# Kernel optimization log

Hardware: AMD Instinct MI355X
Metric: run time of the kernel (lower is better)

## Reference

```python
import jax, jax.numpy as jnp
import numpy as np

N_NODES = 102400   # 256 graphs x 400 nodes
N_EDGES = 1638400  # avg degree 16
C_IN = 128
C_OUT = 128
N_SAGE = 3         # gnn_num
G = 256            # num graphs
M = 400            # nodes per graph (equal-sized -> to_dense_batch is a reshape)


def setup_inputs() -> dict:
    key = jax.random.key(0)
    ks = jax.random.split(key, 6)
    x = jax.random.normal(ks[0], (N_NODES, C_IN), dtype=jnp.float32)
    edge_index = jax.random.randint(ks[1], (2, N_EDGES), 0, N_NODES, dtype=jnp.int32)
    # nodes sorted by graph id, equal graph sizes (matches to_dense_batch assumptions)
    batch = (jnp.arange(N_NODES, dtype=jnp.int32) // M)
    s_in = 1.0 / np.sqrt(C_IN)
    s_out = 1.0 / np.sqrt(C_OUT)
    W_g = jax.random.normal(ks[2], (C_IN, C_OUT), dtype=jnp.float32) * s_in
    b_g = jnp.zeros((C_OUT,), dtype=jnp.float32)
    W_l = jax.random.normal(ks[3], (N_SAGE, C_OUT, C_OUT), dtype=jnp.float32) * s_out  # neighbor lin
    b_l = jnp.zeros((N_SAGE, C_OUT), dtype=jnp.float32)
    W_r = jax.random.normal(ks[4], (N_SAGE, C_OUT, C_OUT), dtype=jnp.float32) * s_out  # root lin (no bias in PyG)
    return {"x": x, "W_g": W_g, "b_g": b_g, "W_l": W_l, "b_l": b_l,
            "W_r": W_r, "edge_index": edge_index, "batch": batch}


def _gcn_conv(x, W, b, src, dst):
    # PyG GCNConv: h = x W; add self loops; norm = d^{-1/2}_src * d^{-1/2}_dst,
    # deg = in-degree at dst counting the self loop; aggregate at dst; add bias.
    h = x @ W                                                     # [N, C_out]
    ones = jnp.ones((N_EDGES,), dtype=h.dtype)
    deg = jax.ops.segment_sum(ones, dst, num_segments=N_NODES) + 1.0
    dinv = jax.lax.rsqrt(deg)                                     # [N]
    norm = dinv[src] * dinv[dst]                                  # [E]
    agg = jax.ops.segment_sum(h[src] * norm[:, None], dst, num_segments=N_NODES)
    agg = agg + h * (dinv * dinv)[:, None]                        # self-loop term
    return agg + b


def _sage_conv(x, W_l, b_l, W_r, src, dst):
    # PyG SAGEConv (mean aggr): out = mean_{j in N(i)} x_j @ W_l + b_l + x @ W_r
    ones = jnp.ones((N_EDGES,), dtype=x.dtype)
    cnt = jax.ops.segment_sum(ones, dst, num_segments=N_NODES)
    s = jax.ops.segment_sum(x[src], dst, num_segments=N_NODES)
    mean = s / jnp.maximum(cnt, 1.0)[:, None]
    return mean @ W_l + b_l + x @ W_r


def _to_dense(x):
    # equal-sized graphs with nodes sorted by batch -> to_dense_batch == reshape
    return x.reshape(G, M, C_OUT)


def reference(x, W_g, b_g, W_l, b_l, W_r, edge_index, batch):
    src, dst = edge_index[0], edge_index[1]
    x = jax.nn.relu(_gcn_conv(x, W_g, b_g, src, dst))
    outs = [_to_dense(x)]
    for i in range(N_SAGE):
        x = jax.nn.relu(_sage_conv(x, W_l[i], b_l[i], W_r[i], src, dst))
        outs.append(_to_dense(x))
    return jnp.stack(outs)  # [N_SAGE+1, G, M, C_OUT]
```

## Files before the change

kernel.cpp:

```cpp
#include <hip/hip_runtime.h>

#define C 128
#define SLOT 64
typedef __attribute__((ext_vector_type(8))) short bf16x8;
typedef __attribute__((ext_vector_type(4))) float f32x4;

__device__ __forceinline__ unsigned short f2bf_rtn(float f) {
    unsigned u = __float_as_uint(f);
    return (unsigned short)((u + 0x7fff + ((u >> 16) & 1)) >> 16);
}
__device__ __forceinline__ float bflo(unsigned u) { return __uint_as_float(u << 16); }
__device__ __forceinline__ float bfhi(unsigned u) { return __uint_as_float(u & 0xffff0000u); }

__device__ __forceinline__ void gload_lds16(const unsigned short* g, unsigned short* l) {
    __builtin_amdgcn_global_load_lds(
        (const __attribute__((address_space(1))) void*)g,
        (__attribute__((address_space(3))) void*)l, 16, 0, 0);
}


__global__ void deg_fill_kernel(const int* __restrict__ ei, int* __restrict__ deg,
                                int* __restrict__ csr, int E) {
    int e = blockIdx.x * blockDim.x + threadIdx.x;
    if (e < E) {
        int d = ei[E + e];
        int r = atomicAdd(&deg[d], 1);
        if (r < SLOT) csr[(d << 6) + r] = ei[e];
    }
}

__global__ void prep_kernel(const int* __restrict__ deg, float* __restrict__ dinv,
                            float* __restrict__ cinv, int n) {
    int i = blockIdx.x * blockDim.x + threadIdx.x;
    if (i < n) {
        int d = deg[i];
        dinv[i] = rsqrtf((float)(d + 1));
        cinv[i] = 1.0f / (float)max(d, 1);
    }
}


__device__ __forceinline__ void split_bf16(float w, unsigned short& hb, unsigned short& lb) {
    unsigned u = __float_as_uint(w);
    hb = (unsigned short)(u >> 16);
    float hf = __uint_as_float(u & 0xffff0000u);
    lb = (unsigned short)(__float_as_uint(w - hf) >> 16);
}

__global__ __launch_bounds__(256) void wprep_gcn(const float* __restrict__ Wg,
                                                 unsigned short* __restrict__ dst) {
    int idx = blockIdx.x * 256 + threadIdx.x;
    if (idx >= 2 * 128 * 64) return;
    int k64 = idx & 63, ch = (idx >> 6) & 127, chunk = idx >> 13;
    int k = chunk * 64 + k64;
    unsigned short hb, lb;
    split_bf16(Wg[(size_t)k * 128 + ch], hb, lb);
    int pos = (((k64 >> 3) ^ (ch & 7)) << 3) | (k64 & 7);
    size_t base = ((size_t)chunk * 2) * 8192 + ch * 64 + pos;
    dst[base] = hb;
    dst[base + 8192] = lb;
}

__global__ __launch_bounds__(256) void wprep_fused(const float* __restrict__ Wl,
        const float* __restrict__ Wr, unsigned short* __restrict__ dst) {
    int idx = blockIdx.x * 256 + threadIdx.x;
    if (idx >= 3 * 4 * 128 * 64) return;
    int k64 = idx & 63, ch = (idx >> 6) & 127, chunk = (idx >> 13) & 3, layer = idx >> 15;
    int k = chunk * 64 + k64;
    float w = (k < 128) ? Wl[((size_t)layer * 128 + k) * 128 + ch]
                        : Wr[((size_t)layer * 128 + (k - 128)) * 128 + ch];
    unsigned short hb, lb;
    split_bf16(w, hb, lb);
    int pos = (((k64 >> 3) ^ (ch & 7)) << 3) | (k64 & 7);
    size_t base = (((size_t)layer * 4 + chunk) * 2) * 8192 + ch * 64 + pos;
    dst[base] = hb;
    dst[base + 8192] = lb;
}

template<int FUSED, int WBF>
__global__ __launch_bounds__(256) void gemm_mfma(
        const float* __restrict__ A0f, const unsigned short* __restrict__ Mbf,
        const unsigned short* __restrict__ Wp, const float* __restrict__ bias,
        float* __restrict__ outf, unsigned short* __restrict__ outbf) {
    const int NCHUNK = FUSED ? 4 : 2;
    __shared__ unsigned short Bs[2][128][64];
    unsigned short* BsFlat = &Bs[0][0][0];
    const int t = threadIdx.x;
    const int lane = t & 63;
    const int wv = t >> 6;
    const int rowbase = blockIdx.x * 64 + wv * 16;
    const int arow = rowbase + (lane & 15);
    const int kq = lane >> 4;

    f32x4 acc[8];
#pragma unroll
    for (int f = 0; f < 8; f++) acc[f] = (f32x4){0.f, 0.f, 0.f, 0.f};

#pragma unroll
    for (int c = 0; c < NCHUNK; c++) {
        __syncthreads();
        {
            const unsigned short* srcW = Wp + (size_t)c * 16384;
#pragma unroll
            for (int i = 0; i < 8; i++)
                gload_lds16(srcW + (wv * 8 + i) * 512 + lane * 8,
                            BsFlat + (wv * 8 + i) * 512);
        }
        const bool mside = (FUSED && c < 2);
        bf16x8 Ah[2], Al[2];
#pragma unroll
        for (int j = 0; j < 2; j++) {
            if (mside) {
                Ah[j] = *(const bf16x8*)(Mbf + (size_t)arow * C + c * 64 + j * 32 + kq * 8);
            } else {
                const int kb = (FUSED ? (c - 2) : c) * 64 + j * 32;
                const float* base = A0f + (size_t)arow * C + kb;
                float4 x0 = ((const float4*)base)[kq * 2];
                float4 x1 = ((const float4*)base)[kq * 2 + 1];
                float xv[8] = {x0.x, x0.y, x0.z, x0.w, x1.x, x1.y, x1.z, x1.w};
#pragma unroll
                for (int q = 0; q < 8; q++) {
                    unsigned u = __float_as_uint(xv[q]);
                    Ah[j][q] = (short)(u >> 16);
                    float hf = __uint_as_float(u & 0xffff0000u);
                    Al[j][q] = (short)(__float_as_uint(xv[q] - hf) >> 16);
                }
            }
        }
        __syncthreads();
#pragma unroll
        for (int j = 0; j < 2; j++) {
#pragma unroll
            for (int f = 0; f < 8; f++) {
                const int chh = f * 16 + (lane & 15);
                const int uu = (j * 4 + kq) ^ (lane & 7);
                bf16x8 bh = *(const bf16x8*)&Bs[0][chh][uu * 8];
                bf16x8 bl = *(const bf16x8*)&Bs[1][chh][uu * 8];
                acc[f] = __builtin_amdgcn_mfma_f32_16x16x32_bf16(Ah[j], bh, acc[f], 0, 0, 0);
                if (!mside)
                    acc[f] = __builtin_amdgcn_mfma_f32_16x16x32_bf16(Al[j], bh, acc[f], 0, 0, 0);
                acc[f] = __builtin_amdgcn_mfma_f32_16x16x32_bf16(Ah[j], bl, acc[f], 0, 0, 0);
            }
        }
    }
    const int col = lane & 15;
    const int rq = lane >> 4;
    if (FUSED) {
#pragma unroll
        for (int f = 0; f < 8; f++) {
            const float b = bias[f * 16 + col];
#pragma unroll
            for (int j = 0; j < 4; j++) {
                const size_t o = (size_t)(rowbase + rq * 4 + j) * C + f * 16 + col;
                float v = fmaxf(acc[f][j] + b, 0.f);
                outf[o] = v;
                if (WBF) outbf[o] = f2bf_rtn(v);
            }
        }
    } else {
        float sc[4];
#pragma unroll
        for (int j = 0; j < 4; j++) sc[j] = bias[rowbase + rq * 4 + j];
#pragma unroll
        for (int f = 0; f < 8; f++)
#pragma unroll
            for (int j = 0; j < 4; j++) {
                const size_t o = (size_t)(rowbase + rq * 4 + j) * C + f * 16 + col;
                outbf[o] = f2bf_rtn(acc[f][j] * sc[j]);
            }
    }
}

template<int SELF, int BIASRELU, int WF, int WBF>
__global__ __launch_bounds__(256) void agg_kernel(
        const unsigned short* __restrict__ tbl, const int* __restrict__ csr,
        const int* __restrict__ deg, const float* __restrict__ scale,
        const float* __restrict__ bias, float* __restrict__ outf,
        unsigned short* __restrict__ outbf, int n) {
    const int lane = threadIdx.x & 63;
    const int half = lane >> 5, li = lane & 31;
    const int i = blockIdx.x * 8 + (threadIdx.x >> 6) * 2 + half;
    if (i >= n) return;
    const int dcount = min(deg[i], SLOT);
    const int b = i << 6;
    const int c4 = li * 4;
    float a0 = 0.f, a1 = 0.f, a2 = 0.f, a3 = 0.f;
    for (int base = 0; base < dcount; base += 32) {
        const int cnt = min(32, dcount - base);
        int idx = (base + li < dcount) ? csr[b + base + li] : 0;
        int p = 0;
        for (; p + 4 <= cnt; p += 4) {
            int s0 = __shfl(idx, half * 32 + p);
            int s1 = __shfl(idx, half * 32 + p + 1);
            int s2 = __shfl(idx, half * 32 + p + 2);
            int s3 = __shfl(idx, half * 32 + p + 3);
            uint2 v0 = *(const uint2*)(tbl + (size_t)s0 * C + c4);
            uint2 v1 = *(const uint2*)(tbl + (size_t)s1 * C + c4);
            uint2 v2 = *(const uint2*)(tbl + (size_t)s2 * C + c4);
            uint2 v3 = *(const uint2*)(tbl + (size_t)s3 * C + c4);
            a0 += bflo(v0.x) + bflo(v1.x) + bflo(v2.x) + bflo(v3.x);
            a1 += bfhi(v0.x) + bfhi(v1.x) + bfhi(v2.x) + bfhi(v3.x);
            a2 += bflo(v0.y) + bflo(v1.y) + bflo(v2.y) + bflo(v3.y);
            a3 += bfhi(v0.y) + bfhi(v1.y) + bfhi(v2.y) + bfhi(v3.y);
        }
        for (; p < cnt; p++) {
            int s = __shfl(idx, half * 32 + p);
            uint2 v = *(const uint2*)(tbl + (size_t)s * C + c4);
            a0 += bflo(v.x); a1 += bfhi(v.x);
            a2 += bflo(v.y); a3 += bfhi(v.y);
        }
    }
    if (SELF) {
        uint2 h = *(const uint2*)(tbl + (size_t)i * C + c4);
        a0 += bflo(h.x); a1 += bfhi(h.x);
        a2 += bflo(h.y); a3 += bfhi(h.y);
    }
    const float sc = scale[i];
    a0 *= sc; a1 *= sc; a2 *= sc; a3 *= sc;
    if (BIASRELU) {
        float4 bb = *(const float4*)(bias + c4);
        a0 = fmaxf(a0 + bb.x, 0.f);
        a1 = fmaxf(a1 + bb.y, 0.f);
        a2 = fmaxf(a2 + bb.z, 0.f);
        a3 = fmaxf(a3 + bb.w, 0.f);
    }
    if (WF) {
        float4 r; r.x = a0; r.y = a1; r.z = a2; r.w = a3;
        *(float4*)(outf + (size_t)i * C + c4) = r;
    }
    if (WBF) {
        uint2 pk;
        pk.x = (unsigned)f2bf_rtn(a0) | ((unsigned)f2bf_rtn(a1) << 16);
        pk.y = (unsigned)f2bf_rtn(a2) | ((unsigned)f2bf_rtn(a3) << 16);
        *(uint2*)(outbf + (size_t)i * C + c4) = pk;
    }
}


extern "C" void kernel_launch(void* const* d_in, const int* in_sizes, int n_in,
                              void* d_out, int out_size, void* d_ws, size_t ws_size,
                              hipStream_t stream) {
    const float* x   = (const float*)d_in[0];
    const float* W_g = (const float*)d_in[1];
    const float* b_g = (const float*)d_in[2];
    const float* W_l = (const float*)d_in[3];
    const float* b_l = (const float*)d_in[4];
    const float* W_r = (const float*)d_in[5];
    const int*   ei  = (const int*)d_in[6];

    const int N = in_sizes[0] / C;
    const int E = in_sizes[6] / 2;
    const size_t NC = (size_t)N * C;

    char* ws = (char*)d_ws;
    unsigned short* meanbf = (unsigned short*)ws;
    unsigned short* tblA   = meanbf + NC;
    unsigned short* tblB   = tblA + NC;
    int* deg  = (int*)(tblB + NC);
    float* dinv = (float*)(deg + N);
    float* cinv = dinv + N;
    unsigned short* wsWg = (unsigned short*)(cinv + N);
    unsigned short* wsWf = wsWg + 32768;

    float* out0 = (float*)d_out;
    int* csr = (int*)(out0 + 3 * NC);

    hipMemsetAsync(deg, 0, (size_t)N * 4, stream);
    deg_fill_kernel<<<(E + 255) / 256, 256, 0, stream>>>(ei, deg, csr, E);
    prep_kernel<<<(N + 255) / 256, 256, 0, stream>>>(deg, dinv, cinv, N);
    wprep_gcn<<<64, 256, 0, stream>>>(W_g, wsWg);
    wprep_fused<<<384, 256, 0, stream>>>(W_l, W_r, wsWf);

    gemm_mfma<0, 1><<<N / 64, 256, 0, stream>>>(x, nullptr, wsWg, dinv, nullptr, tblA);
    agg_kernel<1, 1, 1, 1><<<(N + 7) / 8, 256, 0, stream>>>(tblA, csr, deg, dinv,
                                                            b_g, out0, tblB, N);

    const unsigned short* tin[3] = {tblB, tblA, tblB};
    unsigned short* tout[3] = {tblA, tblB, nullptr};
    for (int l = 0; l < 3; l++) {
        const float* xin = out0 + (size_t)l * NC;
        float* yout      = out0 + (size_t)(l + 1) * NC;
        agg_kernel<0, 0, 0, 1><<<(N + 7) / 8, 256, 0, stream>>>(
            tin[l], csr, deg, cinv, nullptr, nullptr, meanbf, N);
        if (l < 2)
            gemm_mfma<1, 1><<<N / 64, 256, 0, stream>>>(xin, meanbf,
                wsWf + (size_t)l * 65536, b_l + (size_t)l * C, yout, tout[l]);
        else
            gemm_mfma<1, 0><<<N / 64, 256, 0, stream>>>(xin, meanbf,
                wsWf + (size_t)l * 65536, b_l + (size_t)l * C, yout, nullptr);
    }
}
```

Measured before the change: 481.6 us.

## Split CSR build into rank+scatter fused with GCN GEMM; read bf16 root features in SAGE GEMM

The degree-count kernel now records only each edge's atomic rank. The CSR scatter runs on the even blocks of a new kernel whose odd blocks compute the GCN linear transform, so the irregular scatter overlaps with MFMA work. The SAGE GEMM now takes the root features from the bf16 table already produced for aggregation, instead of reloading fp32 activations and splitting them into hi/lo parts. This removes one MFMA per step and half the activation read traffic, at the cost of bf16 precision on the root term.

New measurement: 456.1 us. -5.3%, faster.

```diff
diff --git a/kernel.cpp b/kernel.cpp
--- a/kernel.cpp
+++ b/kernel.cpp
@@ -19,14 +19,10 @@
 }
 
 
-__global__ void deg_fill_kernel(const int* __restrict__ ei, int* __restrict__ deg,
-                                int* __restrict__ csr, int E) {
+__global__ void deg_rank_kernel(const int* __restrict__ ei, int* __restrict__ deg,
+                                int* __restrict__ rank, int E) {
     int e = blockIdx.x * blockDim.x + threadIdx.x;
-    if (e < E) {
-        int d = ei[E + e];
-        int r = atomicAdd(&deg[d], 1);
-        if (r < SLOT) csr[(d << 6) + r] = ei[e];
-    }
+    if (e < E) rank[e] = atomicAdd(&deg[ei[E + e]], 1);
 }
 
 __global__ void prep_kernel(const int* __restrict__ deg, float* __restrict__ dinv,
@@ -77,12 +73,97 @@
     dst[base + 8192] = lb;
 }
 
-template<int FUSED, int WBF>
-__global__ __launch_bounds__(256) void gemm_mfma(
-        const float* __restrict__ A0f, const unsigned short* __restrict__ Mbf,
+__global__ __launch_bounds__(256) void csr_gemm_kernel(
+        const int* __restrict__ ei, const int* __restrict__ rank,
+        int* __restrict__ csr, int E,
+        const float* __restrict__ x, const unsigned short* __restrict__ Wp,
+        const float* __restrict__ dinv, unsigned short* __restrict__ outbf) {
+    __shared__ unsigned short Bs[2][128][64];
+    const int b2 = blockIdx.x >> 1;
+    const int t = threadIdx.x;
+
+    if (!(blockIdx.x & 1)) {
+        const int base = b2 * 1024 + t * 4;
+        int4 s4 = *(const int4*)(ei + base);
+        int4 d4 = *(const int4*)(ei + E + base);
+        int4 r4 = *(const int4*)(rank + base);
+        if (r4.x < SLOT) csr[(d4.x << 6) + r4.x] = s4.x;
+        if (r4.y < SLOT) csr[(d4.y << 6) + r4.y] = s4.y;
+        if (r4.z < SLOT) csr[(d4.z << 6) + r4.z] = s4.z;
+        if (r4.w < SLOT) csr[(d4.w << 6) + r4.w] = s4.w;
+        return;
+    }
+
+    unsigned short* BsFlat = &Bs[0][0][0];
+    const int lane = t & 63;
+    const int wv = t >> 6;
+    const int rowbase = b2 * 64 + wv * 16;
+    const int arow = rowbase + (lane & 15);
+    const int kq = lane >> 4;
+
+    f32x4 acc[8];
+#pragma unroll
+    for (int f = 0; f < 8; f++) acc[f] = (f32x4){0.f, 0.f, 0.f, 0.f};
+
+#pragma unroll
+    for (int c = 0; c < 2; c++) {
+        __syncthreads();
+        {
+            const unsigned short* srcW = Wp + (size_t)c * 16384;
+#pragma unroll
+            for (int i = 0; i < 8; i++)
+                gload_lds16(srcW + (wv * 8 + i) * 512 + lane * 8,
+                            BsFlat + (wv * 8 + i) * 512);
+        }
+        bf16x8 Ah[2], Al[2];
+#pragma unroll
+        for (int j = 0; j < 2; j++) {
+            const float* base = x + (size_t)arow * C + c * 64 + j * 32;
+            float4 x0 = ((const float4*)base)[kq * 2];
+            float4 x1 = ((const float4*)base)[kq * 2 + 1];
+            float xv[8] = {x0.x, x0.y, x0.z, x0.w, x1.x, x1.y, x1.z, x1.w};
+#pragma unroll
+            for (int q = 0; q < 8; q++) {
+                unsigned u = __float_as_uint(xv[q]);
+                Ah[j][q] = (short)(u >> 16);
+                float hf = __uint_as_float(u & 0xffff0000u);
+                Al[j][q] = (short)(__float_as_uint(xv[q] - hf) >> 16);
+            }
+        }
+        __syncthreads();
+#pragma unroll
+        for (int j = 0; j < 2; j++) {
+#pragma unroll
+            for (int f = 0; f < 8; f++) {
+                const int chh = f * 16 + (lane & 15);
+                const int uu = (j * 4 + kq) ^ (lane & 7);
+                bf16x8 bh = *(const bf16x8*)&Bs[0][chh][uu * 8];
+                bf16x8 bl = *(const bf16x8*)&Bs[1][chh][uu * 8];
+                acc[f] = __builtin_amdgcn_mfma_f32_16x16x32_bf16(Ah[j], bh, acc[f], 0, 0, 0);
+                acc[f] = __builtin_amdgcn_mfma_f32_16x16x32_bf16(Al[j], bh, acc[f], 0, 0, 0);
+                acc[f] = __builtin_amdgcn_mfma_f32_16x16x32_bf16(Ah[j], bl, acc[f], 0, 0, 0);
+            }
+        }
+    }
+    const int col = lane & 15;
+    const int rq = lane >> 4;
+    float sc[4];
+#pragma unroll
+    for (int j = 0; j < 4; j++) sc[j] = dinv[rowbase + rq * 4 + j];
+#pragma unroll
+    for (int f = 0; f < 8; f++)
+#pragma unroll
+        for (int j = 0; j < 4; j++) {
+            const size_t o = (size_t)(rowbase + rq * 4 + j) * C + f * 16 + col;
+            outbf[o] = f2bf_rtn(acc[f][j] * sc[j]);
+        }
+}
+
+template<int WBF>
+__global__ __launch_bounds__(256) void gemm_sage(
+        const unsigned short* __restrict__ Xbf, const unsigned short* __restrict__ Mbf,
         const unsigned short* __restrict__ Wp, const float* __restrict__ bias,
         float* __restrict__ outf, unsigned short* __restrict__ outbf) {
-    const int NCHUNK = FUSED ? 4 : 2;
     __shared__ unsigned short Bs[2][128][64];
     unsigned short* BsFlat = &Bs[0][0][0];
     const int t = threadIdx.x;
@@ -97,7 +178,7 @@
     for (int f = 0; f < 8; f++) acc[f] = (f32x4){0.f, 0.f, 0.f, 0.f};
 
 #pragma unroll
-    for (int c = 0; c < NCHUNK; c++) {
+    for (int c = 0; c < 4; c++) {
         __syncthreads();
         {
             const unsigned short* srcW = Wp + (size_t)c * 16384;
@@ -106,27 +187,11 @@
                 gload_lds16(srcW + (wv * 8 + i) * 512 + lane * 8,
                             BsFlat + (wv * 8 + i) * 512);
         }
-        const bool mside = (FUSED && c < 2);
-        bf16x8 Ah[2], Al[2];
-#pragma unroll
-        for (int j = 0; j < 2; j++) {
-            if (mside) {
-                Ah[j] = *(const bf16x8*)(Mbf + (size_t)arow * C + c * 64 + j * 32 + kq * 8);
-            } else {
-                const int kb = (FUSED ? (c - 2) : c) * 64 + j * 32;
-                const float* base = A0f + (size_t)arow * C + kb;
-                float4 x0 = ((const float4*)base)[kq * 2];
-                float4 x1 = ((const float4*)base)[kq * 2 + 1];
-                float xv[8] = {x0.x, x0.y, x0.z, x0.w, x1.x, x1.y, x1.z, x1.w};
-#pragma unroll
-                for (int q = 0; q < 8; q++) {
-                    unsigned u = __float_as_uint(xv[q]);
-                    Ah[j][q] = (short)(u >> 16);
-                    float hf = __uint_as_float(u & 0xffff0000u);
-                    Al[j][q] = (short)(__float_as_uint(xv[q] - hf) >> 16);
-                }
-            }
-        }
+        const unsigned short* tab = (c < 2) ? Mbf : Xbf;
+        bf16x8 Ah[2];
+#pragma unroll
+        for (int j = 0; j < 2; j++)
+            Ah[j] = *(const bf16x8*)(tab + (size_t)arow * C + (c & 1) * 64 + j * 32 + kq * 8);
         __syncthreads();
 #pragma unroll
         for (int j = 0; j < 2; j++) {
@@ -137,37 +202,22 @@
                 bf16x8 bh = *(const bf16x8*)&Bs[0][chh][uu * 8];
                 bf16x8 bl = *(const bf16x8*)&Bs[1][chh][uu * 8];
                 acc[f] = __builtin_amdgcn_mfma_f32_16x16x32_bf16(Ah[j], bh, acc[f], 0, 0, 0);
-                if (!mside)
-                    acc[f] = __builtin_amdgcn_mfma_f32_16x16x32_bf16(Al[j], bh, acc[f], 0, 0, 0);
                 acc[f] = __builtin_amdgcn_mfma_f32_16x16x32_bf16(Ah[j], bl, acc[f], 0, 0, 0);
             }
         }
     }
     const int col = lane & 15;
     const int rq = lane >> 4;
-    if (FUSED) {
-#pragma unroll
-        for (int f = 0; f < 8; f++) {
-            const float b = bias[f * 16 + col];
-#pragma unroll
-            for (int j = 0; j < 4; j++) {
-                const size_t o = (size_t)(rowbase + rq * 4 + j) * C + f * 16 + col;
-                float v = fmaxf(acc[f][j] + b, 0.f);
-                outf[o] = v;
-                if (WBF) outbf[o] = f2bf_rtn(v);
-            }
-        }
-    } else {
-        float sc[4];
-#pragma unroll
-        for (int j = 0; j < 4; j++) sc[j] = bias[rowbase + rq * 4 + j];
-#pragma unroll
-        for (int f = 0; f < 8; f++)
-#pragma unroll
-            for (int j = 0; j < 4; j++) {
-                const size_t o = (size_t)(rowbase + rq * 4 + j) * C + f * 16 + col;
-                outbf[o] = f2bf_rtn(acc[f][j] * sc[j]);
-            }
+#pragma unroll
+    for (int f = 0; f < 8; f++) {
+        const float b = bias[f * 16 + col];
+#pragma unroll
+        for (int j = 0; j < 4; j++) {
+            const size_t o = (size_t)(rowbase + rq * 4 + j) * C + f * 16 + col;
+            float v = fmaxf(acc[f][j] + b, 0.f);
+            outf[o] = v;
+            if (WBF) outbf[o] = f2bf_rtn(v);
+        }
     }
 }
 
@@ -254,6 +304,7 @@
 
     char* ws = (char*)d_ws;
     unsigned short* meanbf = (unsigned short*)ws;
+    int* rank = (int*)meanbf;
     unsigned short* tblA   = meanbf + NC;
     unsigned short* tblB   = tblA + NC;
     int* deg  = (int*)(tblB + NC);
@@ -266,27 +317,28 @@
     int* csr = (int*)(out0 + 3 * NC);
 
     hipMemsetAsync(deg, 0, (size_t)N * 4, stream);
-    deg_fill_kernel<<<(E + 255) / 256, 256, 0, stream>>>(ei, deg, csr, E);
+    deg_rank_kernel<<<(E + 255) / 256, 256, 0, stream>>>(ei, deg, rank, E);
     prep_kernel<<<(N + 255) / 256, 256, 0, stream>>>(deg, dinv, cinv, N);
     wprep_gcn<<<64, 256, 0, stream>>>(W_g, wsWg);
     wprep_fused<<<384, 256, 0, stream>>>(W_l, W_r, wsWf);
 
-    gemm_mfma<0, 1><<<N / 64, 256, 0, stream>>>(x, nullptr, wsWg, dinv, nullptr, tblA);
+    csr_gemm_kernel<<<2 * (N / 64), 256, 0, stream>>>(ei, rank, csr, E,
+                                                      x, wsWg, dinv, tblA);
+
     agg_kernel<1, 1, 1, 1><<<(N + 7) / 8, 256, 0, stream>>>(tblA, csr, deg, dinv,
                                                             b_g, out0, tblB, N);
 
     const unsigned short* tin[3] = {tblB, tblA, tblB};
     unsigned short* tout[3] = {tblA, tblB, nullptr};
     for (int l = 0; l < 3; l++) {
-        const float* xin = out0 + (size_t)l * NC;
-        float* yout      = out0 + (size_t)(l + 1) * NC;
+        float* yout = out0 + (size_t)(l + 1) * NC;
         agg_kernel<0, 0, 0, 1><<<(N + 7) / 8, 256, 0, stream>>>(
             tin[l], csr, deg, cinv, nullptr, nullptr, meanbf, N);
         if (l < 2)
-            gemm_mfma<1, 1><<<N / 64, 256, 0, stream>>>(xin, meanbf,
+            gemm_sage<1><<<N / 64, 256, 0, stream>>>(tin[l], meanbf,
                 wsWf + (size_t)l * 65536, b_l + (size_t)l * C, yout, tout[l]);
         else
-            gemm_mfma<1, 0><<<N / 64, 256, 0, stream>>>(xin, meanbf,
+            gemm_sage<0><<<N / 64, 256, 0, stream>>>(tin[l], meanbf,
                 wsWf + (size_t)l * 65536, b_l + (size_t)l * C, yout, nullptr);
     }
 }
```
